# Optimization experiments

Hardware: AMD Instinct MI355X
Metric: run time of the kernel (lower is better)

Reference implementation:

```python
import jax, jax.numpy as jnp
import numpy as np
import math

HEAD_DIM = 128
NUM_HEADS = 16
ROPE_BASE = 10000.0


def _rope(x, st_pos):
    # x: [B, S, H, hd], interleaved even/odd rotation as in the torch module
    S, hd = x.shape[1], x.shape[3]
    theta = 1.0 / (ROPE_BASE ** (jnp.arange(0, hd, 2, dtype=jnp.float32) / hd))  # [hd/2]
    pos = jnp.arange(st_pos, st_pos + S, dtype=jnp.float32)[:, None]             # [S,1]
    ang = pos * theta                                                            # [S, hd/2]
    sin = jnp.sin(ang)[None, :, None, :]
    cos = jnp.cos(ang)[None, :, None, :]
    xe, xo = x[..., 0::2], x[..., 1::2]
    re = xe * cos - xo * sin
    ro = xe * sin + xo * cos
    # re-interleave: stack pairs then flatten last two dims
    return jnp.stack([re, ro], axis=-1).reshape(x.shape)


def setup_inputs() -> dict:
    key = jax.random.key(0)
    ks = jax.random.split(key, 6)
    B, S, D = 4, 2048, 2048
    scale = 1.0 / math.sqrt(D)
    x = jax.random.normal(ks[0], (B, S, D), dtype=jnp.float32)
    # causal additive mask (prefill)
    mask = jnp.where(jnp.tril(jnp.ones((S, S), dtype=bool)), 0.0, -1e9).astype(jnp.float32)
    Wq = jax.random.normal(ks[1], (D, NUM_HEADS * HEAD_DIM), dtype=jnp.float32) * scale
    Wk = jax.random.normal(ks[2], (D, NUM_HEADS * HEAD_DIM), dtype=jnp.float32) * scale
    Wv = jax.random.normal(ks[3], (D, NUM_HEADS * HEAD_DIM), dtype=jnp.float32) * scale
    Wo = jax.random.normal(ks[4], (NUM_HEADS * HEAD_DIM, D), dtype=jnp.float32) * scale
    return {"x": x, "mask": mask, "Wq": Wq, "Wk": Wk, "Wv": Wv, "Wo": Wo, "st_pos": 0}


def reference(x, mask, Wq, Wk, Wv, Wo, st_pos):
    B, S, D = x.shape
    H, hd = NUM_HEADS, HEAD_DIM
    q = (x @ Wq).reshape(B, S, H, hd)
    k = (x @ Wk).reshape(B, S, H, hd)
    v = (x @ Wv).reshape(B, S, H, hd)
    q = _rope(q, st_pos)
    k = _rope(k, st_pos)
    # st_pos=0 prefill: cache slice == current k, v; n_rep == 1 (n_kv_heads=num_heads)
    scores = jnp.einsum('bqhd,bkhd->bhqk', q, k) / math.sqrt(hd)
    if mask is not None:
        scores = scores + mask
    attn = jax.nn.softmax(scores, axis=-1)
    a = jnp.einsum('bhqk,bkhd->bqhd', attn, v).reshape(B, S, H * hd)
    return a @ Wo
```

## Files before the change

### kernel.cpp

```cpp
#include <hip/hip_runtime.h>
#include <hip/hip_fp16.h>

typedef _Float16 f16;
typedef __attribute__((ext_vector_type(2))) _Float16 f16x2;
typedef __attribute__((ext_vector_type(4))) _Float16 f16x4v;
typedef __attribute__((ext_vector_type(8))) _Float16 f16x8;
typedef __attribute__((ext_vector_type(4))) float f32x4;
typedef __attribute__((ext_vector_type(4))) int i32x4;

#define DEV __device__ __forceinline__

static constexpr int S_ = 2048;
static constexpr int D_ = 2048;
static constexpr int H_ = 16;
static constexpr int HD_ = 128;
static constexpr int B_ = 4;
static constexpr int QKV_ST = 6144;

typedef const __attribute__((address_space(1))) void* gptr_t;
typedef __attribute__((address_space(3))) void* lptr_t;

DEV void gl_lds16(const void* gsrc, void* lds) {
  __builtin_amdgcn_global_load_lds((gptr_t)gsrc, (lptr_t)lds, 16, 0, 0);
}

DEV int cvt_pk_i32(float a, float b) {
  return __builtin_bit_cast(int, __builtin_amdgcn_cvt_pkrtz(a, b));
}

__global__ __launch_bounds__(256) void cvt_f32_to_f16(const float* __restrict__ in,
                                                      f16* __restrict__ out, long n) {
  long i0 = ((long)blockIdx.x * 256 + threadIdx.x) * 4;
  long stride = (long)gridDim.x * 256 * 4;
  for (long i = i0; i < n; i += stride) {
    float4 v = *(const float4*)(in + i);
    f16x4v o;
    o[0] = (f16)v.x; o[1] = (f16)v.y; o[2] = (f16)v.z; o[3] = (f16)v.w;
    *(f16x4v*)(out + i) = o;
  }
}

__global__ __launch_bounds__(256) void wtrans4(const float* __restrict__ W0, const float* __restrict__ W1,
                                               const float* __restrict__ W2, const float* __restrict__ W3,
                                               f16* __restrict__ Wt) {
  __shared__ float tile[32][33];
  int wi = blockIdx.y;
  const float* W = wi == 0 ? W0 : wi == 1 ? W1 : wi == 2 ? W2 : W3;
  f16* dst = Wt + (size_t)wi * D_ * D_;
  int bx = blockIdx.x & 63, by = blockIdx.x >> 6;
  int r0 = by << 5, c0 = bx << 5;
  int tx = threadIdx.x & 31, ty = threadIdx.x >> 5;
#pragma unroll
  for (int i = 0; i < 4; i++) {
    int r = ty + i * 8;
    tile[r][tx] = W[(size_t)(r0 + r) * D_ + c0 + tx];
  }
  __syncthreads();
#pragma unroll
  for (int i = 0; i < 4; i++) {
    int r = ty + i * 8;
    dst[(size_t)(c0 + r) * D_ + r0 + tx] = (f16)tile[tx][r];
  }
}

DEV f16x8 lds_frag(const f16* half, int row, int s, int lg) {
  int byte = row * 128 + s * 64 + lg * 16;
  byte ^= (row & 7) << 4;
  return *(const f16x8*)((const char*)half + byte);
}

template <typename CT>
__global__ __launch_bounds__(512, 2) void gemm8(const f16* __restrict__ A, const f16* __restrict__ Bt,
                                                CT* __restrict__ C, int M, int N, int K,
                                                int lda, int ldc, long subB, long subC) {
  __shared__ alignas(16) f16 As[2][2][128 * 64];
  __shared__ alignas(16) f16 Bs[2][2][128 * 64];
  int nbx = N >> 8;
  int nwg = (M >> 8) * nbx;
  int bid = blockIdx.x;
  int wi = bid / nwg;
  int bidl = bid - wi * nwg;
  Bt += (size_t)wi * subB;
  C += (size_t)wi * subC;
  int wg = (bidl & 7) * (nwg >> 3) + (bidl >> 3);
  int bx = wg % nbx, by = wg / nbx;
  int tid = threadIdx.x, w = tid >> 6, l = tid & 63;
  int wm = w >> 2, wn = w & 3, lg = l >> 4, ln = l & 15;
  int nt = K >> 6;
  const f16* Ab = A + (size_t)(by * 256) * lda;
  const f16* Bb = Bt + (size_t)(bx * 256) * K;

  auto stageA = [&](const f16* src0, int kt, f16* dst) {
#pragma unroll
    for (int j = 0; j < 2; j++) {
      int c = j * 8 + w;
      int row = c * 8 + (l >> 3);
      int scol = ((l & 7) ^ (row & 7)) << 3;
      gl_lds16(src0 + (size_t)row * lda + kt * 64 + scol, (char*)dst + c * 1024);
    }
  };
  auto stageB = [&](const f16* src0, int kt, f16* dst) {
#pragma unroll
    for (int j = 0; j < 2; j++) {
      int c = j * 8 + w;
      int row = c * 8 + (l >> 3);
      int scol = ((l & 7) ^ (row & 7)) << 3;
      gl_lds16(src0 + (size_t)row * K + kt * 64 + scol, (char*)dst + c * 1024);
    }
  };

  f32x4 acc[8][4] = {};

  stageA(Ab, 0, As[0][0]);
  stageA(Ab + (size_t)128 * lda, 0, As[0][1]);
  stageB(Bb, 0, Bs[0][0]);
  stageB(Bb + (size_t)128 * K, 0, Bs[0][1]);

  for (int t = 0; t < nt; t++) {
    asm volatile("s_waitcnt vmcnt(0)" ::: "memory");
    __builtin_amdgcn_s_barrier();
    asm volatile("" ::: "memory");
    const f16* Ah = As[t & 1][wm];
    const f16* Bh = Bs[t & 1][wn >> 1];
    int br0 = (wn & 1) * 64;
    f16x8 alo[4], ahi[4], b0[4], b1[4];
#pragma unroll
    for (int i = 0; i < 4; i++) b0[i] = lds_frag(Bh, br0 + i * 16 + ln, 0, lg);
#pragma unroll
    for (int i = 0; i < 4; i++) b1[i] = lds_frag(Bh, br0 + i * 16 + ln, 1, lg);
#pragma unroll
    for (int i = 0; i < 4; i++) alo[i] = lds_frag(Ah, i * 16 + ln, 0, lg);
#pragma unroll
    for (int i = 0; i < 4; i++) ahi[i] = lds_frag(Ah, 64 + i * 16 + ln, 0, lg);
    if (t + 1 < nt) {
      stageA(Ab, t + 1, As[(t + 1) & 1][0]);
      stageA(Ab + (size_t)128 * lda, t + 1, As[(t + 1) & 1][1]);
      stageB(Bb, t + 1, Bs[(t + 1) & 1][0]);
      stageB(Bb + (size_t)128 * K, t + 1, Bs[(t + 1) & 1][1]);
    }
    __builtin_amdgcn_s_setprio(1);
#pragma unroll
    for (int mi = 0; mi < 4; mi++)
#pragma unroll
      for (int ni = 0; ni < 4; ni++) {
        acc[mi][ni] = __builtin_amdgcn_mfma_f32_16x16x32_f16(alo[mi], b0[ni], acc[mi][ni], 0, 0, 0);
        acc[mi + 4][ni] = __builtin_amdgcn_mfma_f32_16x16x32_f16(ahi[mi], b0[ni], acc[mi + 4][ni], 0, 0, 0);
      }
    __builtin_amdgcn_s_setprio(0);
#pragma unroll
    for (int i = 0; i < 4; i++) alo[i] = lds_frag(Ah, i * 16 + ln, 1, lg);
#pragma unroll
    for (int i = 0; i < 4; i++) ahi[i] = lds_frag(Ah, 64 + i * 16 + ln, 1, lg);
    __builtin_amdgcn_s_setprio(1);
#pragma unroll
    for (int mi = 0; mi < 4; mi++)
#pragma unroll
      for (int ni = 0; ni < 4; ni++) {
        acc[mi][ni] = __builtin_amdgcn_mfma_f32_16x16x32_f16(alo[mi], b1[ni], acc[mi][ni], 0, 0, 0);
        acc[mi + 4][ni] = __builtin_amdgcn_mfma_f32_16x16x32_f16(ahi[mi], b1[ni], acc[mi + 4][ni], 0, 0, 0);
      }
    __builtin_amdgcn_s_setprio(0);
    asm volatile("" ::: "memory");
  }

  int row0 = by * 256 + wm * 128;
  int col0 = bx * 256 + wn * 64;
#pragma unroll
  for (int mi = 0; mi < 8; mi++)
#pragma unroll
    for (int ni = 0; ni < 4; ni++)
#pragma unroll
      for (int r4 = 0; r4 < 4; r4++) {
        int row = row0 + mi * 16 + lg * 4 + r4;
        int col = col0 + ni * 16 + ln;
        float o = acc[mi][ni][r4];
        if constexpr (sizeof(CT) == 2) {
          float oo = __shfl_xor(o, 1);
          if (!(ln & 1)) {
            f16x2 pp; pp[0] = (f16)o; pp[1] = (f16)oo;
            *(f16x2*)(&C[(size_t)row * ldc + col]) = pp;
          }
        } else {
          C[(size_t)row * ldc + col] = o;
        }
      }
}

__global__ __launch_bounds__(256) void rope_table(float2* __restrict__ tab, const int* __restrict__ st) {
  int i = blockIdx.x * 256 + threadIdx.x;
  int s = i >> 6, j = i & 63;
  float theta = powf(10000.f, -(float)j / 64.f);
  float ang = (float)(s + st[0]) * theta;
  tab[i] = make_float2(cosf(ang), sinf(ang));
}

__global__ __launch_bounds__(256) void rope_apply_k(f16* __restrict__ QKV, const float2* __restrict__ tab,
                                                    long npairs) {
  long i0 = (long)blockIdx.x * 256 + threadIdx.x;
  long stride = (long)gridDim.x * 256;
  for (long p = i0; p < npairs; p += stride) {
    long row = p >> 10;
    int jp = (int)(p & 1023);
    int s = (int)(row & (S_ - 1));
    float2 cs = tab[s * 64 + (jp & 63)];
    f16* px = QKV + row * QKV_ST + 2048 + 2 * jp;
    f16x2 v = *(const f16x2*)px;
    float xe = (float)v[0], xo = (float)v[1];
    float re = xe * cs.x - xo * cs.y;
    float ro = xe * cs.y + xo * cs.x;
    f16x2 o; o[0] = (f16)re; o[1] = (f16)ro;
    *(f16x2*)px = o;
  }
}

__global__ __launch_bounds__(256) void vtrans2(const f16* __restrict__ QKV, f16* __restrict__ VT2) {
  __shared__ alignas(16) f16 tile[64 * 128];
  int t = blockIdx.x, bh = blockIdx.y, b = bh >> 4, h = bh & 15;
  int tid = threadIdx.x, w = tid >> 6, l = tid & 63, lg = l >> 4, ln = l & 15;
  const f16* src = QKV + (size_t)(b * S_ + t * 64) * QKV_ST + 4096 + h * HD_;
#pragma unroll
  for (int i = 0; i < 4; i++) {
    int idx = i * 256 + tid;
    int r = idx >> 4, c8 = idx & 15;
    int c8s = c8 ^ ((r >> 3) & 3);
    *(f16x8*)(&tile[r * 128 + c8s * 8]) = *(const f16x8*)(src + (size_t)r * QKV_ST + c8 * 8);
  }
  __syncthreads();
  f16* dst = VT2 + (size_t)(bh * 32 + t) * 16 * 512;
#pragma unroll
  for (int ci = 0; ci < 4; ci++) {
    int c = w * 4 + ci;
    int nj = c >> 1, kk = c & 1;
    f16x8 v;
#pragma unroll
    for (int e = 0; e < 8; e++) {
      int r = 16 * (2 * kk + (e >> 2)) + 4 * lg + (e & 3);
      int col = nj * 16 + ln;
      int c8s = (col >> 3) ^ ((r >> 3) & 3);
      v[e] = tile[r * 128 + c8s * 8 + (col & 7)];
    }
    *(f16x8*)(dst + (size_t)c * 512 + l * 8) = v;
  }
}

__global__ __launch_bounds__(512, 4) void attn(f16* __restrict__ QKV, const f16* __restrict__ VT2,
                                               const float2* __restrict__ tab) {
  __shared__ alignas(16) f16 kls[2][2][64 * 128];
  int id = blockIdx.x;
  int r8 = id & 7, j = id >> 3;
  int u = j & 7, g = j >> 3;
  int bh = r8 + (g << 3);
  int b = bh >> 4, h = bh & 15;
  int tid = threadIdx.x, w = tid >> 6, l = tid & 63, lg = l >> 4, ln = l & 15;

  const float QSCALE = 0.12751744910173355f;
  const f16* kp = QKV + (size_t)(b * S_) * QKV_ST + 2048 + h * HD_;
  const f16* vp2 = VT2 + (size_t)bh * 32 * 16 * 512;

  auto stageK = [&](int buf, int half, int kv0) {
#pragma unroll
    for (int jj = 0; jj < 2; jj++) {
      int i = jj * 8 + w;
      int byte = i * 1024 + 16 * l;
      int r = byte >> 8;
      int c = (((byte >> 4) & 15) - r) & 15;
      gl_lds16(kp + (size_t)(kv0 + r) * QKV_ST + c * 8, (char*)kls[buf][half] + i * 1024);
    }
  };

#pragma unroll 1
  for (int pi = 0; pi < 2; pi++) {
    int qsel = pi ? u : 15 - u;
    int q0 = qsel << 7;
    int qrow = q0 + w * 16 + ln;
    f16* qp = QKV + (size_t)(b * S_ + qrow) * QKV_ST + h * HD_;
    const float2* tq = tab + (size_t)qrow * 64;
    f16x8 qf[4];
#pragma unroll
    for (int kc = 0; kc < 4; kc++) {
      f16x8 q = *(const f16x8*)(qp + kc * 32 + lg * 8);
#pragma unroll
      for (int p = 0; p < 4; p++) {
        float2 cs = tq[kc * 16 + lg * 4 + p];
        float e0 = (float)q[2 * p], e1 = (float)q[2 * p + 1];
        q[2 * p] = (f16)((e0 * cs.x - e1 * cs.y) * QSCALE);
        q[2 * p + 1] = (f16)((e0 * cs.y + e1 * cs.x) * QSCALE);
      }
      qf[kc] = q;
    }

    float m = -1e30f, lsum = 0.f;
    f32x4 oacc[8] = {};

    int np = qsel + 1;
    int nt64 = 2 * qsel + 2;
    if (pi) __syncthreads();
    stageK(0, 0, 0);
    stageK(0, 1, 64);
#pragma unroll 1
    for (int p = 0; p < np; p++) {
      __syncthreads();
      if (p + 1 < np) {
        stageK((p + 1) & 1, 0, (2 * p + 2) << 6);
        stageK((p + 1) & 1, 1, (2 * p + 3) << 6);
      }
#pragma unroll 1
      for (int ii = 0; ii < 2; ii++) {
        int t = 2 * p + ii;
        int kv0 = t << 6;
        if (kv0 > q0 + w * 16 + 15) continue;
        const f16* kb = kls[p & 1][ii];
        const f16* vt = vp2 + (size_t)t * 16 * 512;

        f32x4 sf[4];
        __builtin_amdgcn_s_setprio(1);
#pragma unroll
        for (int ni = 0; ni < 4; ni++) {
          int n = ni * 16 + ln;
          f32x4 s = {0.f, 0.f, 0.f, 0.f};
#pragma unroll
          for (int kc = 0; kc < 4; kc++) {
            int mch = kc * 4 + lg;
            f16x8 kf = *(const f16x8*)(&kb[n * 128 + (((mch + n) & 15) << 3)]);
            s = __builtin_amdgcn_mfma_f32_16x16x32_f16(kf, qf[kc], s, 0, 0, 0);
          }
          sf[ni] = s;
        }
        __builtin_amdgcn_s_setprio(0);

        f16x8 vfa[8];
#pragma unroll
        for (int c = 0; c < 8; c++) vfa[c] = *(const f16x8*)(vt + c * 512 + l * 8);

        if (t >= nt64 - 2) {
#pragma unroll
          for (int ni = 0; ni < 4; ni++) {
            int kvg = kv0 + ni * 16 + lg * 4;
#pragma unroll
            for (int r4 = 0; r4 < 4; r4++)
              if (kvg + r4 > qrow) sf[ni][r4] = -1e30f;
          }
        }
        float pm = fmaxf(fmaxf(fmaxf(sf[0][0], sf[0][1]), fmaxf(sf[0][2], sf[0][3])),
                         fmaxf(fmaxf(sf[1][0], sf[1][1]), fmaxf(sf[1][2], sf[1][3])));
        pm = fmaxf(pm, fmaxf(fmaxf(fmaxf(sf[2][0], sf[2][1]), fmaxf(sf[2][2], sf[2][3])),
                             fmaxf(fmaxf(sf[3][0], sf[3][1]), fmaxf(sf[3][2], sf[3][3]))));
        pm = fmaxf(pm, __shfl_xor(pm, 16));
        pm = fmaxf(pm, __shfl_xor(pm, 32));
        float scl = 1.f;
        bool defer = __all(pm <= m + 8.f);
        if (!defer) {
          float mn = fmaxf(m, pm);
          scl = __builtin_amdgcn_exp2f(m - mn);
          m = mn;
        }
        float rsum = 0.f;
#pragma unroll
        for (int ni = 0; ni < 4; ni++)
#pragma unroll
          for (int r4 = 0; r4 < 4; r4++) {
            float pv = __builtin_amdgcn_exp2f(sf[ni][r4] - m);
            sf[ni][r4] = pv;
            rsum += pv;
          }
        lsum = lsum * scl + rsum;

        if (!defer) {
#pragma unroll
          for (int nj = 0; nj < 8; nj++)
#pragma unroll
            for (int r4 = 0; r4 < 4; r4++) oacc[nj][r4] *= scl;
        }

        f16x8 pa[2];
#pragma unroll
        for (int kk = 0; kk < 2; kk++) {
          i32x4 wv;
          wv.x = cvt_pk_i32(sf[2 * kk][0], sf[2 * kk][1]);
          wv.y = cvt_pk_i32(sf[2 * kk][2], sf[2 * kk][3]);
          wv.z = cvt_pk_i32(sf[2 * kk + 1][0], sf[2 * kk + 1][1]);
          wv.w = cvt_pk_i32(sf[2 * kk + 1][2], sf[2 * kk + 1][3]);
          pa[kk] = __builtin_bit_cast(f16x8, wv);
        }

        __builtin_amdgcn_s_setprio(1);
#pragma unroll
        for (int kk = 0; kk < 2; kk++)
#pragma unroll
          for (int nj = 0; nj < 4; nj++)
            oacc[nj] = __builtin_amdgcn_mfma_f32_16x16x32_f16(vfa[nj * 2 + kk], pa[kk], oacc[nj], 0, 0, 0);
#pragma unroll
        for (int njb = 0; njb < 2; njb++) {
          f16x8 vf[4];
#pragma unroll
          for (int jj = 0; jj < 2; jj++)
#pragma unroll
            for (int kk = 0; kk < 2; kk++)
              vf[jj * 2 + kk] = *(const f16x8*)(vt + (size_t)(((4 + njb * 2 + jj) * 2 + kk) * 512) + l * 8);
#pragma unroll
          for (int kk = 0; kk < 2; kk++)
#pragma unroll
            for (int jj = 0; jj < 2; jj++)
              oacc[4 + njb * 2 + jj] = __builtin_amdgcn_mfma_f32_16x16x32_f16(
                  vf[jj * 2 + kk], pa[kk], oacc[4 + njb * 2 + jj], 0, 0, 0);
        }
        __builtin_amdgcn_s_setprio(0);
      }
    }

    lsum += __shfl_xor(lsum, 16);
    lsum += __shfl_xor(lsum, 32);
    float inv = 1.f / lsum;
#pragma unroll
    for (int nj = 0; nj < 8; nj++) {
      f16x4v ov;
#pragma unroll
      for (int r4 = 0; r4 < 4; r4++) ov[r4] = (f16)(oacc[nj][r4] * inv);
      *(f16x4v*)(qp + nj * 16 + lg * 4) = ov;
    }
  }
}

extern "C" void kernel_launch(void* const* d_in, const int* in_sizes, int n_in,
                              void* d_out, int out_size, void* d_ws, size_t ws_size,
                              hipStream_t stream) {
  (void)in_sizes; (void)n_in; (void)out_size; (void)ws_size;
  const float* x = (const float*)d_in[0];
  const float* Wq = (const float*)d_in[2];
  const float* Wk = (const float*)d_in[3];
  const float* Wv = (const float*)d_in[4];
  const float* Wo = (const float*)d_in[5];
  const int* stp = (const int*)d_in[6];
  float* out = (float*)d_out;

  const size_t MS = (size_t)B_ * S_;
  f16* xh = (f16*)d_ws;
  f16* wqt = xh + MS * D_;
  f16* wot = wqt + (size_t)3 * D_ * D_;
  f16* qkv = wot + (size_t)D_ * D_;
  float2* tab = (float2*)(qkv + MS * (size_t)QKV_ST);
  f16* vt2 = xh;

  cvt_f32_to_f16<<<16384, 256, 0, stream>>>(x, xh, (long)(MS * D_));
  wtrans4<<<dim3(4096, 4), 256, 0, stream>>>(Wq, Wk, Wv, Wo, wqt);
  gemm8<f16><<<768, 512, 0, stream>>>(xh, wqt, qkv, 8192, 2048, 2048, 2048, QKV_ST,
                                      (long)D_ * D_, 2048);
  rope_table<<<512, 256, 0, stream>>>(tab, stp);
  rope_apply_k<<<4096, 256, 0, stream>>>(qkv, tab, (long)(MS * 1024));
  vtrans2<<<dim3(32, 64), 256, 0, stream>>>(qkv, vt2);
  attn<<<512, 512, 0, stream>>>(qkv, vt2, tab);
  gemm8<float><<<256, 512, 0, stream>>>(qkv, wot, out, 8192, 2048, 2048, QKV_ST, 2048, 0, 0);
}
```

Measured before the change: 433.5 us.

## Fuse V transpose into QKV GEMM epilogue and drop vtrans2 kernel

The QKV GEMM epilogue for the V third (wi==2) now writes V directly in the MFMA-fragment-friendly transposed layout inside the QKV buffer's V columns, so the separate vtrans2 kernel and its extra read/write pass over V are removed. The attention kernel reads V fragments from that in-place layout via a new index function. Separately, the LDS fragment loads in the GEMM main loop are moved after issuing the next tile's global-to-LDS prefetch, so the prefetch is issued earlier. The epilogue store pattern for V becomes scattered 8-byte writes, which may coalesce less well than the original row stores.

```diff
diff --git a/kernel.cpp b/kernel.cpp
--- a/kernel.cpp
+++ b/kernel.cpp
@@ -120,24 +120,24 @@
     asm volatile("s_waitcnt vmcnt(0)" ::: "memory");
     __builtin_amdgcn_s_barrier();
     asm volatile("" ::: "memory");
-    const f16* Ah = As[t & 1][wm];
-    const f16* Bh = Bs[t & 1][wn >> 1];
-    int br0 = (wn & 1) * 64;
-    f16x8 alo[4], ahi[4], b0[4], b1[4];
-#pragma unroll
-    for (int i = 0; i < 4; i++) b0[i] = lds_frag(Bh, br0 + i * 16 + ln, 0, lg);
-#pragma unroll
-    for (int i = 0; i < 4; i++) b1[i] = lds_frag(Bh, br0 + i * 16 + ln, 1, lg);
-#pragma unroll
-    for (int i = 0; i < 4; i++) alo[i] = lds_frag(Ah, i * 16 + ln, 0, lg);
-#pragma unroll
-    for (int i = 0; i < 4; i++) ahi[i] = lds_frag(Ah, 64 + i * 16 + ln, 0, lg);
     if (t + 1 < nt) {
       stageA(Ab, t + 1, As[(t + 1) & 1][0]);
       stageA(Ab + (size_t)128 * lda, t + 1, As[(t + 1) & 1][1]);
       stageB(Bb, t + 1, Bs[(t + 1) & 1][0]);
       stageB(Bb + (size_t)128 * K, t + 1, Bs[(t + 1) & 1][1]);
     }
+    const f16* Ah = As[t & 1][wm];
+    const f16* Bh = Bs[t & 1][wn >> 1];
+    int br0 = (wn & 1) * 64;
+    f16x8 alo[4], ahi[4], b0[4], b1[4];
+#pragma unroll
+    for (int i = 0; i < 4; i++) b0[i] = lds_frag(Bh, br0 + i * 16 + ln, 0, lg);
+#pragma unroll
+    for (int i = 0; i < 4; i++) b1[i] = lds_frag(Bh, br0 + i * 16 + ln, 1, lg);
+#pragma unroll
+    for (int i = 0; i < 4; i++) alo[i] = lds_frag(Ah, i * 16 + ln, 0, lg);
+#pragma unroll
+    for (int i = 0; i < 4; i++) ahi[i] = lds_frag(Ah, 64 + i * 16 + ln, 0, lg);
     __builtin_amdgcn_s_setprio(1);
 #pragma unroll
     for (int mi = 0; mi < 4; mi++)
@@ -165,6 +165,26 @@
 
   int row0 = by * 256 + wm * 128;
   int col0 = bx * 256 + wn * 64;
+  if constexpr (sizeof(CT) == 2) {
+    if (wi == 2) {
+#pragma unroll
+      for (int mi = 0; mi < 8; mi++)
+#pragma unroll
+        for (int ni = 0; ni < 4; ni++) {
+          f16x4v pv;
+#pragma unroll
+          for (int r4 = 0; r4 < 4; r4++) pv[r4] = (f16)acc[mi][ni][r4];
+          int row = row0 + mi * 16 + lg * 4;
+          int col = col0 + ni * 16 + ln;
+          int bh = ((row >> 11) << 4) + ((col >> 7) & 15);
+          int tt = (row & 2047) >> 6;
+          int cc = (((col & 127) >> 4) << 1) + ((mi >> 1) & 1);
+          long L = ((long)(bh * 32 + tt) << 13) + cc * 512 + l * 8 + 4 * (mi & 1);
+          *(f16x4v*)(&C[(size_t)(L >> 11) * ldc + (L & 2047)]) = pv;
+        }
+      return;
+    }
+  }
 #pragma unroll
   for (int mi = 0; mi < 8; mi++)
 #pragma unroll
@@ -213,38 +233,7 @@
   }
 }
 
-__global__ __launch_bounds__(256) void vtrans2(const f16* __restrict__ QKV, f16* __restrict__ VT2) {
-  __shared__ alignas(16) f16 tile[64 * 128];
-  int t = blockIdx.x, bh = blockIdx.y, b = bh >> 4, h = bh & 15;
-  int tid = threadIdx.x, w = tid >> 6, l = tid & 63, lg = l >> 4, ln = l & 15;
-  const f16* src = QKV + (size_t)(b * S_ + t * 64) * QKV_ST + 4096 + h * HD_;
-#pragma unroll
-  for (int i = 0; i < 4; i++) {
-    int idx = i * 256 + tid;
-    int r = idx >> 4, c8 = idx & 15;
-    int c8s = c8 ^ ((r >> 3) & 3);
-    *(f16x8*)(&tile[r * 128 + c8s * 8]) = *(const f16x8*)(src + (size_t)r * QKV_ST + c8 * 8);
-  }
-  __syncthreads();
-  f16* dst = VT2 + (size_t)(bh * 32 + t) * 16 * 512;
-#pragma unroll
-  for (int ci = 0; ci < 4; ci++) {
-    int c = w * 4 + ci;
-    int nj = c >> 1, kk = c & 1;
-    f16x8 v;
-#pragma unroll
-    for (int e = 0; e < 8; e++) {
-      int r = 16 * (2 * kk + (e >> 2)) + 4 * lg + (e & 3);
-      int col = nj * 16 + ln;
-      int c8s = (col >> 3) ^ ((r >> 3) & 3);
-      v[e] = tile[r * 128 + c8s * 8 + (col & 7)];
-    }
-    *(f16x8*)(dst + (size_t)c * 512 + l * 8) = v;
-  }
-}
-
-__global__ __launch_bounds__(512, 4) void attn(f16* __restrict__ QKV, const f16* __restrict__ VT2,
-                                               const float2* __restrict__ tab) {
+__global__ __launch_bounds__(512, 4) void attn(f16* __restrict__ QKV, const float2* __restrict__ tab) {
   __shared__ alignas(16) f16 kls[2][2][64 * 128];
   int id = blockIdx.x;
   int r8 = id & 7, j = id >> 3;
@@ -255,7 +244,8 @@
 
   const float QSCALE = 0.12751744910173355f;
   const f16* kp = QKV + (size_t)(b * S_) * QKV_ST + 2048 + h * HD_;
-  const f16* vp2 = VT2 + (size_t)bh * 32 * 16 * 512;
+  const f16* vb = QKV + 4096;
+  int vrow0 = bh * 128;
 
   auto stageK = [&](int buf, int half, int kv0) {
 #pragma unroll
@@ -266,6 +256,9 @@
       int c = (((byte >> 4) & 15) - r) & 15;
       gl_lds16(kp + (size_t)(kv0 + r) * QKV_ST + c * 8, (char*)kls[buf][half] + i * 1024);
     }
+  };
+  auto vload = [&](int t, int c) -> f16x8 {
+    return *(const f16x8*)(vb + (size_t)(vrow0 + t * 4 + (c >> 2)) * QKV_ST + (c & 3) * 512 + l * 8);
   };
 
 #pragma unroll 1
@@ -310,7 +303,6 @@
         int kv0 = t << 6;
         if (kv0 > q0 + w * 16 + 15) continue;
         const f16* kb = kls[p & 1][ii];
-        const f16* vt = vp2 + (size_t)t * 16 * 512;
 
         f32x4 sf[4];
         __builtin_amdgcn_s_setprio(1);
@@ -330,7 +322,7 @@
 
         f16x8 vfa[8];
 #pragma unroll
-        for (int c = 0; c < 8; c++) vfa[c] = *(const f16x8*)(vt + c * 512 + l * 8);
+        for (int c = 0; c < 8; c++) vfa[c] = vload(t, c);
 
         if (t >= nt64 - 2) {
 #pragma unroll
@@ -396,7 +388,7 @@
           for (int jj = 0; jj < 2; jj++)
 #pragma unroll
             for (int kk = 0; kk < 2; kk++)
-              vf[jj * 2 + kk] = *(const f16x8*)(vt + (size_t)(((4 + njb * 2 + jj) * 2 + kk) * 512) + l * 8);
+              vf[jj * 2 + kk] = vload(t, (4 + njb * 2 + jj) * 2 + kk);
 #pragma unroll
           for (int kk = 0; kk < 2; kk++)
 #pragma unroll
@@ -439,7 +431,6 @@
   f16* wot = wqt + (size_t)3 * D_ * D_;
   f16* qkv = wot + (size_t)D_ * D_;
   float2* tab = (float2*)(qkv + MS * (size_t)QKV_ST);
-  f16* vt2 = xh;
 
   cvt_f32_to_f16<<<16384, 256, 0, stream>>>(x, xh, (long)(MS * D_));
   wtrans4<<<dim3(4096, 4), 256, 0, stream>>>(Wq, Wk, Wv, Wo, wqt);
@@ -447,7 +438,6 @@
                                       (long)D_ * D_, 2048);
   rope_table<<<512, 256, 0, stream>>>(tab, stp);
   rope_apply_k<<<4096, 256, 0, stream>>>(qkv, tab, (long)(MS * 1024));
-  vtrans2<<<dim3(32, 64), 256, 0, stream>>>(qkv, vt2);
-  attn<<<512, 512, 0, stream>>>(qkv, vt2, tab);
+  attn<<<512, 512, 0, stream>>>(qkv, tab);
   gemm8<float><<<256, 512, 0, stream>>>(qkv, wot, out, 8192, 2048, 2048, QKV_ST, 2048, 0, 0);
 }
```

After: 447.9 us. 3.3% more time.
